# Optimization experiments

Measured on AMD Instinct MI355X. Metric: run time of the kernel, lower is better.

## Reference

```python
import jax, jax.numpy as jnp
import numpy as np

N_HEADS = 16
D_MODEL = 1024
TOTAL = 8192
N_SEQ = 8
SEQ_LEN = TOTAL // N_SEQ


def setup_inputs() -> dict:
    key = jax.random.key(0)
    ks = jax.random.split(key, 12)
    f = jnp.float32
    d = D_MODEL
    inp = {
        "query": jax.random.normal(ks[0], (TOTAL, d), f),
        "key": jax.random.normal(ks[1], (TOTAL, d), f),
        "value": jax.random.normal(ks[2], (TOTAL, d), f),
        "seq_lengths_q": jnp.full((N_SEQ,), SEQ_LEN, jnp.int64 if jax.config.jax_enable_x64 else jnp.int32),
        "seq_lengths_kv": jnp.full((N_SEQ,), SEQ_LEN, jnp.int64 if jax.config.jax_enable_x64 else jnp.int32),
        "Wq": jax.random.normal(ks[3], (d, d), f) * 0.02,
        "bq": jnp.zeros((d,), f),
        "Wk": jax.random.normal(ks[4], (d, d), f) * 0.02,
        "bk": jnp.zeros((d,), f),
        "Wv": jax.random.normal(ks[5], (d, d), f) * 0.02,
        "bv": jnp.zeros((d,), f),
        "Wo": jax.random.normal(ks[6], (d, d), f) * 0.02,
        "bo": jnpp if False else jnp.zeros((d,), f),
    }
    return inp


def reference(query, key, value, seq_lengths_q, seq_lengths_kv, Wq, bq, Wk, bk, Wv, bv, Wo, bo):
    Tq, d = query.shape
    Tkv = key.shape[0]
    H = N_HEADS
    Dh = d // H
    B = seq_lengths_q.shape[0]
    Lq = Tq // B  # equal-length packed sequences
    Lkv = Tkv // B
    scale = 1.0 / jnp.sqrt(jnp.asarray(Dh, query.dtype))

    # torch Linear: x @ W.T + b
    Q = (query @ Wq.T + bq).reshape(H, Tq, Dh)   # NOTE: raw view, no transpose
    K = (key @ Wk.T + bk).reshape(H, Tkv, Dh)    # (replicates original's view semantics)
    V = (value @ Wv.T + bv).reshape(H, Tkv, Dh)

    # Block-diagonal mask over equal-length sequences == per-block attention.
    Qb = Q.reshape(H, B, Lq, Dh)
    Kb = K.reshape(H, B, Lkv, Dh)
    Vb = V.reshape(H, B, Lkv, Dh)

    scores = jnp.einsum("hbqd,hbkd->hbqk", Qb, Kb) * scale  # [H,B,Lq,Lkv]
    probs = jax.nn.softmax(scores, axis=-1)
    attn = jnp.einsum("hbqk,hbkd->hbqd", probs, Vb)          # [H,B,Lq,Dh]

    attn = attn.reshape(H, Tq, Dh).reshape(Tq, d)  # matches .view(total_q, d_model)
    out = attn @ Wo.T + bo
    return out
```

## Files before the change

kernel.cpp:

```cpp
#include <hip/hip_runtime.h>
#include <hip/hip_bf16.h>

#define TOTAL   8192
#define DMODEL  1024
#define NHEADS  16
#define NSEQ    8
#define DH      64

typedef float  f32x4 __attribute__((ext_vector_type(4)));
typedef short  s16x8 __attribute__((ext_vector_type(8)));
typedef unsigned short u16;
typedef u16    u16x8 __attribute__((ext_vector_type(8)));

__device__ __forceinline__ u16 f2bf_rne(float x) {
  union { float f; unsigned u; } v; v.f = x;
  unsigned r = v.u + 0x7FFFu + ((v.u >> 16) & 1u);
  return (u16)(r >> 16);
}

__device__ __forceinline__ void async_cp16(const u16* g, u16* l) {
  __builtin_amdgcn_global_load_lds(
      (const __attribute__((address_space(1))) unsigned int*)g,
      (__attribute__((address_space(3))) unsigned int*)l, 16, 0, 0);
}

__device__ __forceinline__ void cvt8_one(const float* __restrict__ src,
                                         u16* __restrict__ dst, long i) {
  float4 a = *reinterpret_cast<const float4*>(src + i);
  float4 b = *reinterpret_cast<const float4*>(src + i + 4);
  u16x8 o;
  o[0] = f2bf_rne(a.x); o[1] = f2bf_rne(a.y); o[2] = f2bf_rne(a.z); o[3] = f2bf_rne(a.w);
  o[4] = f2bf_rne(b.x); o[5] = f2bf_rne(b.y); o[6] = f2bf_rne(b.z); o[7] = f2bf_rne(b.w);
  *reinterpret_cast<u16x8*>(dst + i) = o;
}

__global__ __launch_bounds__(256) void cvt8(const float* __restrict__ src,
                                            u16* __restrict__ dst) {
  cvt8_one(src, dst, ((long)blockIdx.x * 256 + threadIdx.x) * 8);
}

__global__ __launch_bounds__(256) void cvt8_w4(const float* __restrict__ w0,
                                               const float* __restrict__ w1,
                                               const float* __restrict__ w2,
                                               const float* __restrict__ w3,
                                               u16* __restrict__ dst) {
  const float* srcs[4] = {w0, w1, w2, w3};
  cvt8_one(srcs[blockIdx.y], dst + (long)blockIdx.y * (DMODEL * (long)DMODEL),
           ((long)blockIdx.x * 256 + threadIdx.x) * 8);
}

__global__ __launch_bounds__(256) void cvt8_x3(const float* __restrict__ x0,
                                               const float* __restrict__ x1,
                                               const float* __restrict__ x2,
                                               u16* __restrict__ dst) {
  const float* srcs[3] = {x0, x1, x2};
  cvt8_one(srcs[blockIdx.y], dst + (long)blockIdx.y * (TOTAL * (long)DMODEL),
           ((long)blockIdx.x * 256 + threadIdx.x) * 8);
}

template<bool OUT_BF16>
__device__ __forceinline__ void gemm_core(const u16* __restrict__ A,
                                          const u16* __restrict__ B,
                                          const float* __restrict__ bias,
                                          void* __restrict__ Cp,
                                          long bm0, long bn0,
                                          u16* As, u16* Bs) {
  const int tid  = threadIdx.x;
  const int lane = tid & 63;
  const int wv   = tid >> 6;
  const int quad = lane >> 4;
  const int m16  = lane & 15;
  const int wm   = (wv & 1) * 64;
  const int wn   = (wv >> 1) * 64;
  const int srow = lane >> 2;
  const int sk8  = (lane & 3) * 8;

  f32x4 acc[4][4] = {};
  const u16* Abase = A + bm0 * DMODEL;
  const u16* Bbase = B + bn0 * DMODEL;

  for (int k0 = 0; k0 < DMODEL; k0 += 32) {
    #pragma unroll
    for (int j = 0; j < 2; j++) {
      const int r   = j * 4 + wv;
      const int row = r * 16 + srow;
      async_cp16(Abase + (long)row * DMODEL + k0 + sk8, &As[r * 512]);
      async_cp16(Bbase + (long)row * DMODEL + k0 + sk8, &Bs[r * 512]);
    }
    __syncthreads();

    s16x8 af[4], bfr[4];
    #pragma unroll
    for (int i = 0; i < 4; i++)
      af[i] = *(const s16x8*)&As[(wm + i * 16 + m16) * 32 + quad * 8];
    #pragma unroll
    for (int j = 0; j < 4; j++)
      bfr[j] = *(const s16x8*)&Bs[(wn + j * 16 + m16) * 32 + quad * 8];
    #pragma unroll
    for (int i = 0; i < 4; i++)
      #pragma unroll
      for (int j = 0; j < 4; j++)
        acc[i][j] = __builtin_amdgcn_mfma_f32_16x16x32_bf16(af[i], bfr[j], acc[i][j], 0, 0, 0);
    __syncthreads();
  }

  #pragma unroll
  for (int j = 0; j < 4; j++) {
    const long col = bn0 + wn + j * 16 + m16;
    const float bj = bias[col];
    #pragma unroll
    for (int i = 0; i < 4; i++) {
      const long row0 = bm0 + wm + i * 16 + quad * 4;
      #pragma unroll
      for (int r = 0; r < 4; r++) {
        float v = acc[i][j][r] + bj;
        if constexpr (OUT_BF16)
          ((u16*)Cp)[(row0 + r) * DMODEL + col] = f2bf_rne(v);
        else
          ((float*)Cp)[(row0 + r) * DMODEL + col] = v;
      }
    }
  }
}

template<bool OUT_BF16>
__global__ __launch_bounds__(256) void gemm_nt_async(const u16* __restrict__ A,
                                                     const u16* __restrict__ B,
                                                     const float* __restrict__ bias,
                                                     void* __restrict__ Cp) {
  __shared__ u16 As[128 * 32];
  __shared__ u16 Bs[128 * 32];
  gemm_core<OUT_BF16>(A, B, bias, Cp,
                      (long)blockIdx.x * 128, (long)blockIdx.y * 128, As, Bs);
}

__global__ __launch_bounds__(256) void gemm_qkv(const u16* __restrict__ X3,
                                                const u16* __restrict__ W3,
                                                const float* __restrict__ bq,
                                                const float* __restrict__ bk,
                                                const float* __restrict__ bv,
                                                u16* __restrict__ QKV) {
  __shared__ u16 As[128 * 32];
  __shared__ u16 Bs[128 * 32];
  const int z = blockIdx.z;
  const float* bias = (z == 0) ? bq : (z == 1) ? bk : bv;
  gemm_core<true>(X3 + (long)z * (TOTAL * (long)DMODEL),
                  W3 + (long)z * (DMODEL * (long)DMODEL),
                  bias,
                  QKV + (long)z * (TOTAL * (long)DMODEL),
                  (long)blockIdx.x * 128, (long)blockIdx.y * 128, As, Bs);
}

__global__ __launch_bounds__(256) void transpose_v(const u16* __restrict__ Vbf,
                                                   u16* __restrict__ Vt) {
  constexpr int TP = 72;
  __shared__ u16 tile[64 * TP];
  const int tid = threadIdx.x;
  const long base = (long)blockIdx.y * 65536;
  const int kt = blockIdx.x;
  {
    int k = tid >> 2, dh0 = (tid & 3) * 16;
    const u16* g = Vbf + base + (long)(kt * 64 + k) * 64 + dh0;
    u16x8 a = ((const u16x8*)g)[0];
    u16x8 b = ((const u16x8*)g)[1];
    #pragma unroll
    for (int i = 0; i < 8; i++) tile[(dh0 + i) * TP + k] = a[i];
    #pragma unroll
    for (int i = 0; i < 8; i++) tile[(dh0 + 8 + i) * TP + k] = b[i];
  }
  __syncthreads();
  {
    int dh = tid >> 2, k0 = (tid & 3) * 16;
    u16x8 a = *(const u16x8*)&tile[dh * TP + k0];
    u16x8 b = *(const u16x8*)&tile[dh * TP + k0 + 8];
    u16* g = Vt + base + (long)dh * 1024 + kt * 64 + k0;
    ((u16x8*)g)[0] = a;
    ((u16x8*)g)[1] = b;
  }
}

__global__ __launch_bounds__(256) void attn_kernel(const u16* __restrict__ Qbf,
                                                   const u16* __restrict__ Kbf,
                                                   const u16* __restrict__ Vt,
                                                   u16* __restrict__ Obf) {
  constexpr int KP = 72;
  __shared__ u16 Ks[64 * KP];
  __shared__ u16 Vs[64 * KP];
  __shared__ u16 Es[4 * 32 * KP];
  const int tid  = threadIdx.x;
  const int lane = tid & 63;
  const int wv   = tid >> 6;
  const int quad = lane >> 4;
  const int m16  = lane & 15;
  const int qt   = blockIdx.y;
  const long base = (long)blockIdx.x * 65536;

  const int qrow0 = qt * 128 + wv * 32;
  s16x8 aq[2][2];
  #pragma unroll
  for (int g = 0; g < 2; g++)
    #pragma unroll
    for (int s = 0; s < 2; s++)
      aq[g][s] = *(const s16x8*)(Qbf + base + (long)(qrow0 + g * 16 + m16) * 64 + s * 32 + quad * 8);

  f32x4 acc_o[2][4] = {};
  f32x4 acc_d[2] = {};

  union { u16x8 u; s16x8 s; } onesu;
  u16 ov = (m16 == 0) ? (u16)0x3F80 : (u16)0;
  #pragma unroll
  for (int i = 0; i < 8; i++) onesu.u[i] = ov;
  const s16x8 bones = onesu.s;

  const float SC = 0.125f * 1.44269504088896340736f;
  const int sr = tid >> 2;
  const int sk = (tid & 3) * 16;

  for (int nt = 0; nt < 16; nt++) {
    {
      const u16* g = Kbf + base + nt * 4096 + (long)sr * 64 + sk;
      u16x8 a = ((const u16x8*)g)[0];
      u16x8 b = ((const u16x8*)g)[1];
      *(u16x8*)&Ks[sr * KP + sk]     = a;
      *(u16x8*)&Ks[sr * KP + sk + 8] = b;
    }
    {
      const u16* g = Vt + base + (long)sr * 1024 + nt * 64 + sk;
      u16x8 a = ((const u16x8*)g)[0];
      u16x8 b = ((const u16x8*)g)[1];
      *(u16x8*)&Vs[sr * KP + sk]     = a;
      *(u16x8*)&Vs[sr * KP + sk + 8] = b;
    }
    __syncthreads();

    #pragma unroll
    for (int n = 0; n < 4; n++) {
      s16x8 bk0 = *(const s16x8*)&Ks[(n * 16 + m16) * KP + quad * 8];
      s16x8 bk1 = *(const s16x8*)&Ks[(n * 16 + m16) * KP + 32 + quad * 8];
      #pragma unroll
      for (int g = 0; g < 2; g++) {
        f32x4 s = {0.f, 0.f, 0.f, 0.f};
        s = __builtin_amdgcn_mfma_f32_16x16x32_bf16(aq[g][0], bk0, s, 0, 0, 0);
        s = __builtin_amdgcn_mfma_f32_16x16x32_bf16(aq[g][1], bk1, s, 0, 0, 0);
        #pragma unroll
        for (int r = 0; r < 4; r++) {
          float e = __builtin_amdgcn_exp2f(s[r] * SC);
          Es[(wv * 32 + g * 16 + quad * 4 + r) * KP + n * 16 + m16] = f2bf_rne(e);
        }
      }
    }
    s16x8 ae[2][2];
    #pragma unroll
    for (int g = 0; g < 2; g++) {
      ae[g][0] = *(const s16x8*)&Es[(wv * 32 + g * 16 + m16) * KP + quad * 8];
      ae[g][1] = *(const s16x8*)&Es[(wv * 32 + g * 16 + m16) * KP + 32 + quad * 8];
    }
    #pragma unroll
    for (int n = 0; n < 4; n++) {
      s16x8 bv0 = *(const s16x8*)&Vs[(n * 16 + m16) * KP + quad * 8];
      s16x8 bv1 = *(const s16x8*)&Vs[(n * 16 + m16) * KP + 32 + quad * 8];
      #pragma unroll
      for (int g = 0; g < 2; g++) {
        acc_o[g][n] = __builtin_amdgcn_mfma_f32_16x16x32_bf16(ae[g][0], bv0, acc_o[g][n], 0, 0, 0);
        acc_o[g][n] = __builtin_amdgcn_mfma_f32_16x16x32_bf16(ae[g][1], bv1, acc_o[g][n], 0, 0, 0);
      }
    }
    #pragma unroll
    for (int g = 0; g < 2; g++) {
      acc_d[g] = __builtin_amdgcn_mfma_f32_16x16x32_bf16(ae[g][0], bones, acc_d[g], 0, 0, 0);
      acc_d[g] = __builtin_amdgcn_mfma_f32_16x16x32_bf16(ae[g][1], bones, acc_d[g], 0, 0, 0);
    }
    __syncthreads();
  }

  #pragma unroll
  for (int g = 0; g < 2; g++)
    #pragma unroll
    for (int r = 0; r < 4; r++) {
      float d = __shfl(acc_d[g][r], lane & 48);
      float rinv = 1.0f / d;
      const long orow = base + (long)(qrow0 + g * 16 + quad * 4 + r) * 64;
      #pragma unroll
      for (int n = 0; n < 4; n++)
        Obf[orow + n * 16 + m16] = f2bf_rne(acc_o[g][n][r] * rinv);
    }
}

extern "C" void kernel_launch(void* const* d_in, const int* in_sizes, int n_in,
                              void* d_out, int out_size, void* d_ws, size_t ws_size,
                              hipStream_t stream) {
  const float* query = (const float*)d_in[0];
  const float* key_  = (const float*)d_in[1];
  const float* value = (const float*)d_in[2];
  const float* Wq = (const float*)d_in[5];
  const float* bq = (const float*)d_in[6];
  const float* Wk = (const float*)d_in[7];
  const float* bk = (const float*)d_in[8];
  const float* Wv = (const float*)d_in[9];
  const float* bv = (const float*)d_in[10];
  const float* Wo = (const float*)d_in[11];
  const float* bo = (const float*)d_in[12];

  char* ws = (char*)d_ws;
  const size_t FUSED_NEED = 104ull << 20;

  if (ws_size >= FUSED_NEED) {
    u16* Wbf = (u16*)(ws);
    u16* QKV = (u16*)(ws + (8l << 20));
    u16* Qbf = QKV;
    u16* Kbf = QKV + 1 * (TOTAL * (long)DMODEL);
    u16* Vbf = QKV + 2 * (TOTAL * (long)DMODEL);
    u16* X3  = (u16*)(ws + (56l << 20));
    u16* Vt  = X3;
    u16* Obf = Vbf;

    cvt8_w4<<<dim3(512, 4), 256, 0, stream>>>(Wq, Wk, Wv, Wo, Wbf);
    cvt8_x3<<<dim3(4096, 3), 256, 0, stream>>>(query, key_, value, X3);
    gemm_qkv<<<dim3(64, 8, 3), 256, 0, stream>>>(X3, Wbf, bq, bk, bv, QKV);
    transpose_v<<<dim3(16, 128), 256, 0, stream>>>(Vbf, Vt);
    attn_kernel<<<dim3(128, 8), 256, 0, stream>>>(Qbf, Kbf, Vt, Obf);
    gemm_nt_async<false><<<dim3(64, 8), 256, 0, stream>>>(Obf, Wbf + 3 * 1048576, bo, (float*)d_out);
  } else {
    u16* Wbf = (u16*)(ws);
    u16* Xbf = (u16*)(ws + (8l << 20));
    u16* Qbf = (u16*)(ws + (24l << 20));
    u16* Kbf = (u16*)(ws + (40l << 20));
    u16* Vbf = (u16*)(ws + (56l << 20));
    u16* Vt  = Xbf;
    u16* Obf = Vbf;

    cvt8_w4<<<dim3(512, 4), 256, 0, stream>>>(Wq, Wk, Wv, Wo, Wbf);
    cvt8<<<4096, 256, 0, stream>>>(query, Xbf);
    gemm_nt_async<true><<<dim3(64, 8), 256, 0, stream>>>(Xbf, Wbf + 0 * 1048576, bq, Qbf);
    cvt8<<<4096, 256, 0, stream>>>(key_, Xbf);
    gemm_nt_async<true><<<dim3(64, 8), 256, 0, stream>>>(Xbf, Wbf + 1 * 1048576, bk, Kbf);
    cvt8<<<4096, 256, 0, stream>>>(value, Xbf);
    gemm_nt_async<true><<<dim3(64, 8), 256, 0, stream>>>(Xbf, Wbf + 2 * 1048576, bv, Vbf);
    transpose_v<<<dim3(16, 128), 256, 0, stream>>>(Vbf, Vt);
    attn_kernel<<<dim3(128, 8), 256, 0, stream>>>(Qbf, Kbf, Vt, Obf);
    gemm_nt_async<false><<<dim3(64, 8), 256, 0, stream>>>(Obf, Wbf + 3 * 1048576, bo, (float*)d_out);
  }
}
```

Baseline: 329.2 us.

## Rewrite projection GEMMs as 256x128 tiles with triple-buffered swizzled LDS pipeline

Replaces the 128x128, 256-thread GEMM core with a 256x128 tile, 512-thread kernel. It adds a three-stage async global-to-LDS pipeline with BK=64, XOR-swizzled LDS to avoid bank conflicts, explicit waitcnt and barriers, setprio around MFMA bursts, and a remapped workgroup order for L2 locality. The goal is to hide global load latency and raise MFMA utilisation in the QKV and output projections. The cost is about 144KB of LDS per block and hand-tuned wait counts, which could limit occupancy or be fragile.

```diff
diff --git a/kernel.cpp b/kernel.cpp
--- a/kernel.cpp
+++ b/kernel.cpp
@@ -59,61 +59,118 @@
 }
 
 template<bool OUT_BF16>
-__device__ __forceinline__ void gemm_core(const u16* __restrict__ A,
-                                          const u16* __restrict__ B,
-                                          const float* __restrict__ bias,
-                                          void* __restrict__ Cp,
-                                          long bm0, long bn0,
-                                          u16* As, u16* Bs) {
+__device__ __forceinline__ void gemm256_core(const u16* __restrict__ A,
+                                             const u16* __restrict__ B,
+                                             const float* __restrict__ bias,
+                                             void* __restrict__ Cp,
+                                             long bm0, long bn0, u16* lds) {
   const int tid  = threadIdx.x;
   const int lane = tid & 63;
   const int wv   = tid >> 6;
   const int quad = lane >> 4;
   const int m16  = lane & 15;
-  const int wm   = (wv & 1) * 64;
-  const int wn   = (wv >> 1) * 64;
-  const int srow = lane >> 2;
-  const int sk8  = (lane & 3) * 8;
+  const int wm   = (wv >> 1) * 64;
+  const int wn   = (wv & 1) * 64;
+
+  const int l8   = lane >> 3;
+  const int slot = (lane & 7) ^ l8;
+  const long g_lane = (long)l8 * DMODEL + slot * 8;
+  const u16* Ap = A + (bm0 + wv * 32) * (long)DMODEL + g_lane;
+  const u16* Bp = B + (bn0 + wv * 16) * (long)DMODEL + g_lane;
+  u16* ldsA = lds + wv * (4 * 512);
+  u16* ldsB = lds + 16384 + wv * (2 * 512);
+
+  const int swz0 = ((quad * 16)      ^ ((m16 & 7) << 4)) >> 1;
+  const int swz1 = ((64 + quad * 16) ^ ((m16 & 7) << 4)) >> 1;
+  const int aro = (wm + m16) * 64;
+  const int bro = 16384 + (wn + m16) * 64;
 
   f32x4 acc[4][4] = {};
-  const u16* Abase = A + bm0 * DMODEL;
-  const u16* Bbase = B + bn0 * DMODEL;
-
-  for (int k0 = 0; k0 < DMODEL; k0 += 32) {
-    #pragma unroll
-    for (int j = 0; j < 2; j++) {
-      const int r   = j * 4 + wv;
-      const int row = r * 16 + srow;
-      async_cp16(Abase + (long)row * DMODEL + k0 + sk8, &As[r * 512]);
-      async_cp16(Bbase + (long)row * DMODEL + k0 + sk8, &Bs[r * 512]);
-    }
-    __syncthreads();
-
-    s16x8 af[4], bfr[4];
-    #pragma unroll
-    for (int i = 0; i < 4; i++)
-      af[i] = *(const s16x8*)&As[(wm + i * 16 + m16) * 32 + quad * 8];
-    #pragma unroll
-    for (int j = 0; j < 4; j++)
-      bfr[j] = *(const s16x8*)&Bs[(wn + j * 16 + m16) * 32 + quad * 8];
-    #pragma unroll
-    for (int i = 0; i < 4; i++)
-      #pragma unroll
-      for (int j = 0; j < 4; j++)
-        acc[i][j] = __builtin_amdgcn_mfma_f32_16x16x32_bf16(af[i], bfr[j], acc[i][j], 0, 0, 0);
-    __syncthreads();
-  }
+
+#define STAGE_A(buf, kt) do {                                       \
+    _Pragma("unroll")                                               \
+    for (int al = 0; al < 4; al++)                                  \
+      async_cp16(Ap + (long)(kt) * 64 + al * (8 * DMODEL),          \
+                 ldsA + (buf) * 24576 + al * 512);                  \
+  } while (0)
+#define STAGE_B(buf, kt) do {                                       \
+    _Pragma("unroll")                                               \
+    for (int bl = 0; bl < 2; bl++)                                  \
+      async_cp16(Bp + (long)(kt) * 64 + bl * (8 * DMODEL),          \
+                 ldsB + (buf) * 24576 + bl * 512);                  \
+  } while (0)
+
+  STAGE_A(0, 0); STAGE_B(0, 0);
+  STAGE_A(1, 1); STAGE_B(1, 1);
 
   #pragma unroll
-  for (int j = 0; j < 4; j++) {
-    const long col = bn0 + wn + j * 16 + m16;
+  for (int t = 0; t < 16; t++) {
+    const int cur = t % 3;
+    const int stg = (t + 2) % 3;
+    if (t < 15) asm volatile("s_waitcnt vmcnt(6)" ::: "memory");
+    else        asm volatile("s_waitcnt vmcnt(0)" ::: "memory");
+    __builtin_amdgcn_s_barrier();
+    asm volatile("" ::: "memory");
+
+    const u16* lb = lds + cur * 24576;
+
+    if (t < 14) STAGE_A(stg, t + 2);
+    s16x8 bf[4][2], af[2][2];
+    #pragma unroll
+    for (int n = 0; n < 4; n++) {
+      bf[n][0] = *(const s16x8*)&lb[bro + n * 1024 + swz0];
+      bf[n][1] = *(const s16x8*)&lb[bro + n * 1024 + swz1];
+    }
+    #pragma unroll
+    for (int i = 0; i < 2; i++) {
+      af[i][0] = *(const s16x8*)&lb[aro + i * 1024 + swz0];
+      af[i][1] = *(const s16x8*)&lb[aro + i * 1024 + swz1];
+    }
+    asm volatile("s_waitcnt lgkmcnt(0)" ::: "memory");
+    __builtin_amdgcn_sched_barrier(0);
+    __builtin_amdgcn_s_setprio(1);
+    #pragma unroll
+    for (int i = 0; i < 2; i++)
+      #pragma unroll
+      for (int n = 0; n < 4; n++) {
+        acc[i][n] = __builtin_amdgcn_mfma_f32_16x16x32_bf16(af[i][0], bf[n][0], acc[i][n], 0, 0, 0);
+        acc[i][n] = __builtin_amdgcn_mfma_f32_16x16x32_bf16(af[i][1], bf[n][1], acc[i][n], 0, 0, 0);
+      }
+    __builtin_amdgcn_s_setprio(0);
+    __builtin_amdgcn_s_barrier();
+
+    if (t < 14) STAGE_B(stg, t + 2);
+    s16x8 ag[2][2];
+    #pragma unroll
+    for (int i = 0; i < 2; i++) {
+      ag[i][0] = *(const s16x8*)&lb[aro + (i + 2) * 1024 + swz0];
+      ag[i][1] = *(const s16x8*)&lb[aro + (i + 2) * 1024 + swz1];
+    }
+    asm volatile("s_waitcnt lgkmcnt(0)" ::: "memory");
+    __builtin_amdgcn_sched_barrier(0);
+    __builtin_amdgcn_s_setprio(1);
+    #pragma unroll
+    for (int i = 0; i < 2; i++)
+      #pragma unroll
+      for (int n = 0; n < 4; n++) {
+        acc[i + 2][n] = __builtin_amdgcn_mfma_f32_16x16x32_bf16(ag[i][0], bf[n][0], acc[i + 2][n], 0, 0, 0);
+        acc[i + 2][n] = __builtin_amdgcn_mfma_f32_16x16x32_bf16(ag[i][1], bf[n][1], acc[i + 2][n], 0, 0, 0);
+      }
+    __builtin_amdgcn_s_setprio(0);
+  }
+#undef STAGE_A
+#undef STAGE_B
+
+  #pragma unroll
+  for (int n = 0; n < 4; n++) {
+    const long col = bn0 + wn + n * 16 + m16;
     const float bj = bias[col];
     #pragma unroll
     for (int i = 0; i < 4; i++) {
       const long row0 = bm0 + wm + i * 16 + quad * 4;
       #pragma unroll
       for (int r = 0; r < 4; r++) {
-        float v = acc[i][j][r] + bj;
+        float v = acc[i][n][r] + bj;
         if constexpr (OUT_BF16)
           ((u16*)Cp)[(row0 + r) * DMODEL + col] = f2bf_rne(v);
         else
@@ -123,32 +180,39 @@
   }
 }
 
+__device__ __forceinline__ void decode_wg(int x, long& bm0, long& bn0) {
+  const int wg = (x & 7) * 32 + (x >> 3);
+  bm0 = (long)(wg >> 3) * 256;
+  bn0 = (long)(wg & 7) * 128;
+}
+
 template<bool OUT_BF16>
-__global__ __launch_bounds__(256) void gemm_nt_async(const u16* __restrict__ A,
+__global__ __launch_bounds__(512, 2) void gemm256_nt(const u16* __restrict__ A,
                                                      const u16* __restrict__ B,
                                                      const float* __restrict__ bias,
                                                      void* __restrict__ Cp) {
-  __shared__ u16 As[128 * 32];
-  __shared__ u16 Bs[128 * 32];
-  gemm_core<OUT_BF16>(A, B, bias, Cp,
-                      (long)blockIdx.x * 128, (long)blockIdx.y * 128, As, Bs);
-}
-
-__global__ __launch_bounds__(256) void gemm_qkv(const u16* __restrict__ X3,
-                                                const u16* __restrict__ W3,
-                                                const float* __restrict__ bq,
-                                                const float* __restrict__ bk,
-                                                const float* __restrict__ bv,
-                                                u16* __restrict__ QKV) {
-  __shared__ u16 As[128 * 32];
-  __shared__ u16 Bs[128 * 32];
-  const int z = blockIdx.z;
+  __shared__ __align__(1024) u16 lds[3 * 24576];
+  long bm0, bn0;
+  decode_wg(blockIdx.x, bm0, bn0);
+  gemm256_core<OUT_BF16>(A, B, bias, Cp, bm0, bn0, lds);
+}
+
+__global__ __launch_bounds__(512, 2) void gemm256_qkv(const u16* __restrict__ X3,
+                                                      const u16* __restrict__ W3,
+                                                      const float* __restrict__ bq,
+                                                      const float* __restrict__ bk,
+                                                      const float* __restrict__ bv,
+                                                      u16* __restrict__ QKV) {
+  __shared__ __align__(1024) u16 lds[3 * 24576];
+  const int z = blockIdx.y;
   const float* bias = (z == 0) ? bq : (z == 1) ? bk : bv;
-  gemm_core<true>(X3 + (long)z * (TOTAL * (long)DMODEL),
-                  W3 + (long)z * (DMODEL * (long)DMODEL),
-                  bias,
-                  QKV + (long)z * (TOTAL * (long)DMODEL),
-                  (long)blockIdx.x * 128, (long)blockIdx.y * 128, As, Bs);
+  long bm0, bn0;
+  decode_wg(blockIdx.x, bm0, bn0);
+  gemm256_core<true>(X3 + (long)z * (TOTAL * (long)DMODEL),
+                     W3 + (long)z * (DMODEL * (long)DMODEL),
+                     bias,
+                     QKV + (long)z * (TOTAL * (long)DMODEL),
+                     bm0, bn0, lds);
 }
 
 __global__ __launch_bounds__(256) void transpose_v(const u16* __restrict__ Vbf,
@@ -316,10 +380,10 @@
 
     cvt8_w4<<<dim3(512, 4), 256, 0, stream>>>(Wq, Wk, Wv, Wo, Wbf);
     cvt8_x3<<<dim3(4096, 3), 256, 0, stream>>>(query, key_, value, X3);
-    gemm_qkv<<<dim3(64, 8, 3), 256, 0, stream>>>(X3, Wbf, bq, bk, bv, QKV);
+    gemm256_qkv<<<dim3(256, 3), 512, 0, stream>>>(X3, Wbf, bq, bk, bv, QKV);
     transpose_v<<<dim3(16, 128), 256, 0, stream>>>(Vbf, Vt);
     attn_kernel<<<dim3(128, 8), 256, 0, stream>>>(Qbf, Kbf, Vt, Obf);
-    gemm_nt_async<false><<<dim3(64, 8), 256, 0, stream>>>(Obf, Wbf + 3 * 1048576, bo, (float*)d_out);
+    gemm256_nt<false><<<dim3(256), 512, 0, stream>>>(Obf, Wbf + 3 * 1048576, bo, (float*)d_out);
   } else {
     u16* Wbf = (u16*)(ws);
     u16* Xbf = (u16*)(ws + (8l << 20));
@@ -331,13 +395,13 @@
 
     cvt8_w4<<<dim3(512, 4), 256, 0, stream>>>(Wq, Wk, Wv, Wo, Wbf);
     cvt8<<<4096, 256, 0, stream>>>(query, Xbf);
-    gemm_nt_async<true><<<dim3(64, 8), 256, 0, stream>>>(Xbf, Wbf + 0 * 1048576, bq, Qbf);
+    gemm256_nt<true><<<dim3(256), 512, 0, stream>>>(Xbf, Wbf + 0 * 1048576, bq, Qbf);
     cvt8<<<4096, 256, 0, stream>>>(key_, Xbf);
-    gemm_nt_async<true><<<dim3(64, 8), 256, 0, stream>>>(Xbf, Wbf + 1 * 1048576, bk, Kbf);
+    gemm256_nt<true><<<dim3(256), 512, 0, stream>>>(Xbf, Wbf + 1 * 1048576, bk, Kbf);
     cvt8<<<4096, 256, 0, stream>>>(value, Xbf);
-    gemm_nt_async<true><<<dim3(64, 8), 256, 0, stream>>>(Xbf, Wbf + 2 * 1048576, bv, Vbf);
+    gemm256_nt<true><<<dim3(256), 512, 0, stream>>>(Xbf, Wbf + 2 * 1048576, bv, Vbf);
     transpose_v<<<dim3(16, 128), 256, 0, stream>>>(Vbf, Vt);
     attn_kernel<<<dim3(128, 8), 256, 0, stream>>>(Qbf, Kbf, Vt, Obf);
-    gemm_nt_async<false><<<dim3(64, 8), 256, 0, stream>>>(Obf, Wbf + 3 * 1048576, bo, (float*)d_out);
-  }
-}
+    gemm256_nt<false><<<dim3(256), 512, 0, stream>>>(Obf, Wbf + 3 * 1048576, bo, (float*)d_out);
+  }
+}
```

Result: faster. 307.0 us (-6.7%).
